# Performance work log

Measured on AMD Instinct MI355X. Metric: run time of the kernel, lower is better.

Reference implementation:

```python
import jax, jax.numpy as jnp
import numpy as np

B, N, FIN, HID, HEADS, LAYERS = 2048, 62, 128, 512, 8, 3
FOUT = HID // HEADS  # 64


def setup_inputs() -> dict:
    key = jax.random.key(0)
    ks = jax.random.split(key, 12)
    x = jax.random.normal(ks[0], (B, N, FIN), dtype=jnp.float32)
    adj = jax.random.randint(ks[1], (B, N, N), 0, 2, dtype=jnp.int32)
    # BatchNorm1d(62) params (eval mode, running stats)
    bn_gamma = jax.random.normal(ks[2], (N,), dtype=jnp.float32) * 0.1 + 1.0
    bn_beta = jax.random.normal(ks[3], (N,), dtype=jnp.float32) * 0.1
    bn_mean = jax.random.normal(ks[4], (N,), dtype=jnp.float32) * 0.1
    bn_var = jax.random.uniform(ks[5], (N,), dtype=jnp.float32, minval=0.5, maxval=1.5)
    # input MLP
    W_mlp = jax.random.normal(ks[6], (FIN, HID), dtype=jnp.float32) / np.sqrt(FIN)
    b_mlp = jnp.zeros((HID,), dtype=jnp.float32)
    # GAT params: one W [HID, FOUT] and one a [2*FOUT] per (layer, head)
    W_gat = jax.random.normal(ks[7], (LAYERS, HEADS, HID, FOUT), dtype=jnp.float32) / np.sqrt(HID)
    a_gat = jax.random.normal(ks[8], (LAYERS, HEADS, 2 * FOUT), dtype=jnp.float32) / np.sqrt(2 * FOUT)
    # output head
    W_out = jax.random.normal(ks[9], (HID, 3), dtype=jnp.float32) / np.sqrt(HID)
    b_out = jnp.zeros((3,), dtype=jnp.float32)
    return {
        "x": x, "adj": adj,
        "bn_gamma": bn_gamma, "bn_beta": bn_beta, "bn_mean": bn_mean, "bn_var": bn_var,
        "W_mlp": W_mlp, "b_mlp": b_mlp,
        "W_gat": W_gat, "a_gat": a_gat,
        "W_out": W_out, "b_out": b_out,
    }


def reference(x, adj, bn_gamma, bn_beta, bn_mean, bn_var, W_mlp, b_mlp, W_gat, a_gat, W_out, b_out):
    eps = 1e-5
    alpha = 0.2  # LeakyReLU slope
    # BatchNorm1d over the node dim (C=62), eval mode
    xb = (x - bn_mean[None, :, None]) * (bn_gamma / jnp.sqrt(bn_var + eps))[None, :, None] + bn_beta[None, :, None]
    h_x = xb @ W_mlp + b_mlp  # [B, N, HID]
    mask = adj > 0  # [B, N, N]
    n_layers, n_heads, _, f_out = W_gat.shape
    for l in range(n_layers):
        # all heads at once: h [H, B, N, FOUT]
        h = jnp.einsum('bnf,hfd->hbnd', h_x, W_gat[l])
        a1 = a_gat[l][:, :f_out]   # multiplies the repeat(1,N,1) part -> h_j
        a2 = a_gat[l][:, f_out:]   # multiplies the repeat(1,1,N) part -> h_i
        f1 = jnp.einsum('hbnd,hd->hbn', h, a1)  # per-node source term
        f2 = jnp.einsum('hbnd,hd->hbn', h, a2)  # per-node dest term
        # e[h,b,i,j] = leaky(a2.h_i + a1.h_j)  (matches cat/repeat layout)
        e = jax.nn.leaky_relu(f2[:, :, :, None] + f1[:, :, None, :], alpha)
        e = jnp.where(mask[None], e, jnp.float32(-9e15))
        # torch F.softmax(attention, dim=1) on [B,N,N] -> axis=2 here (the i axis)
        att = jax.nn.softmax(e, axis=2)
        hp = jnp.einsum('hbij,hbjd->hbid', att, h)
        hp = jax.nn.elu(hp)
        # concat heads on feature dim -> [B, N, HID]
        h_x = jnp.transpose(hp, (1, 2, 0, 3)).reshape(h_x.shape[0], h_x.shape[1], n_heads * f_out)
    pooled = jnp.sum(h_x, axis=1)  # [B, HID]
    logits = pooled @ W_out + b_out  # [B, 3]
    return jax.nn.log_softmax(logits, axis=-1)
```

## Files before the change

### kernel.cpp

```cpp
#include <hip/hip_runtime.h>
#include <cstdint>
#include <cstddef>

#define B_ 2048
#define N_ 62
#define FIN_ 128
#define HID_ 512
#define HEADS_ 8
#define FOUT_ 64
#define LAYERS_ 3
#define M_ (B_*N_)

typedef __bf16 bf16x8 __attribute__((ext_vector_type(8)));
typedef float  f32x4  __attribute__((ext_vector_type(4)));
typedef unsigned short u16;

#define LOG2E 1.4426950408889634f

#if __has_builtin(__builtin_amdgcn_exp2f)
#define EXP2F(x) __builtin_amdgcn_exp2f(x)
#else
#define EXP2F(x) exp2f(x)
#endif
#if __has_builtin(__builtin_amdgcn_logf)
#define LOG2F(x) __builtin_amdgcn_logf(x)
#else
#define LOG2F(x) log2f(x)
#endif

static __device__ __forceinline__ u16 f2bf(float f) {
    union { float f; uint32_t u; } v; v.f = f;
    uint32_t u = v.u;
    return (u16)((u + 0x7fffu + ((u >> 16) & 1u)) >> 16);
}
static __device__ __forceinline__ float bf2f(u16 s) {
    union { uint32_t u; float f; } v; v.u = ((uint32_t)s) << 16;
    return v.f;
}
static __device__ __forceinline__ float rdlane(float v, int l) {
    union { float f; int i; } a, b; a.f = v;
    b.i = __builtin_amdgcn_readlane(a.i, l);
    return b.f;
}

__global__ __launch_bounds__(256) void repack_w(
    const float* __restrict__ Wm, const float* __restrict__ Wg,
    const float* __restrict__ ag,
    u16* __restrict__ wmlp_t, u16* __restrict__ wgat2)
{
    int idx = blockIdx.x * 256 + threadIdx.x;
    const int T1 = HID_ * FIN_;
    const int T2 = LAYERS_ * HEADS_ * 80 * HID_;
    if (idx < T1) {
        int n = idx / FIN_, k = idx % FIN_;
        wmlp_t[idx] = f2bf(Wm[k * HID_ + n]);
    } else if (idx < T1 + T2) {
        int j = idx - T1;
        int lh = j / (80 * HID_);
        int r  = j % (80 * HID_);
        int n = r / HID_, k = r % HID_;
        float v;
        if (n < 64) {
            v = Wg[((size_t)lh * HID_ + k) * FOUT_ + n];
        } else if (n < 66) {
            const float* ap = ag + (size_t)lh * 128 + (n - 64) * 64;
            const float* wrow = Wg + ((size_t)lh * HID_ + k) * FOUT_;
            float s = 0.f;
            for (int d = 0; d < 64; d++) s += wrow[d] * ap[d];
            v = s * LOG2E;
        } else {
            v = 0.f;
        }
        wgat2[j] = f2bf(v);
    }
}

__global__ __launch_bounds__(256) void build_masks(
    const int* __restrict__ adj, uint64_t* __restrict__ masks,
    uint64_t* __restrict__ masksT)
{
    __shared__ uint32_t m32[128];
    const int b = blockIdx.x, tid = threadIdx.x;
    if (tid < 128) m32[tid] = 0;
    __syncthreads();
    const int* a = adj + (size_t)b * N_ * N_;
    for (int idx = tid; idx < N_ * N_; idx += 256) {
        int i = idx / N_, j = idx % N_;
        if (a[idx] > 0) atomicOr(&m32[i * 2 + (j >> 5)], 1u << (j & 31));
    }
    __syncthreads();
    if (tid < 128) ((uint32_t*)(masks + (size_t)b * 64))[tid] = m32[tid];
    if (tid < 64) {
        int j = tid;
        uint64_t c = 0;
        for (int i = 0; i < N_; i++) {
            uint64_t bit = (m32[i * 2 + (j >> 5)] >> (j & 31)) & 1u;
            c |= bit << i;
        }
        masksT[(size_t)b * 64 + j] = c;
    }
}

#define S_IN 520
#define S_T  72
#define S_X  136
#define X0   28160

__global__ __launch_bounds__(512, 4) void gat_fused(
    const float* __restrict__ x,
    const float* __restrict__ bng, const float* __restrict__ bnb,
    const float* __restrict__ bnm, const float* __restrict__ bnv,
    const u16* __restrict__ wmlp_t, const float* __restrict__ bm,
    const u16* __restrict__ wgat2,
    const uint64_t* __restrict__ masks, const uint64_t* __restrict__ masksT,
    const float* __restrict__ Wout, const float* __restrict__ bout,
    float* __restrict__ out)
{
    __shared__ __align__(16) u16 buf[36864];
    __shared__ uint64_t msk[64];
    __shared__ __align__(16) float fstat[1544];
    float* F1 = fstat;
    float* F2 = fstat + 512;
    float* LS = fstat + 1024;

    const int tid = threadIdx.x, b = blockIdx.x;
    const int wave = tid >> 6, lane = tid & 63;
    const int lr = lane & 15, lq = lane >> 4;
    const int w64 = wave * 64;

    const uint64_t cm = masksT[(size_t)b * 64 + lane];
    const uint32_t cml = (uint32_t)cm, cmh = (uint32_t)(cm >> 32);

    {
        const float* xg = x + (size_t)b * N_ * FIN_;
        for (int idx = tid; idx < 2048; idx += 512) {
            int n = idx >> 5, kq = idx & 31;
            ushort4 o = {0, 0, 0, 0};
            if (n < N_) {
                float s = bng[n] * rsqrtf(bnv[n] + 1e-5f);
                float sh = bnb[n] - bnm[n] * s;
                float4 v = *(const float4*)(xg + n * FIN_ + kq * 4);
                o.x = f2bf(v.x * s + sh); o.y = f2bf(v.y * s + sh);
                o.z = f2bf(v.z * s + sh); o.w = f2bf(v.w * s + sh);
            }
            *(ushort4*)&buf[X0 + n * S_X + kq * 4] = o;
        }
        if (tid < 64) msk[tid] = (tid < N_) ? masks[(size_t)b * 64 + tid] : 0ull;
    }
    __syncthreads();

    {
        f32x4 acc[4][4];
#pragma unroll
        for (int mt = 0; mt < 4; mt++)
#pragma unroll
            for (int nt = 0; nt < 4; nt++) acc[mt][nt] = (f32x4){0.f, 0.f, 0.f, 0.f};
        const int c0 = w64;
#pragma unroll
        for (int kt = 0; kt < 4; kt++) {
            int k0 = kt * 32;
            bf16x8 xf[4];
#pragma unroll
            for (int nt = 0; nt < 4; nt++)
                xf[nt] = *(const bf16x8*)&buf[X0 + (nt * 16 + lr) * S_X + k0 + lq * 8];
#pragma unroll
            for (int mt = 0; mt < 4; mt++) {
                bf16x8 wf = *(const bf16x8*)(wmlp_t + (size_t)(c0 + mt * 16 + lr) * FIN_ + k0 + lq * 8);
#pragma unroll
                for (int nt = 0; nt < 4; nt++)
                    acc[mt][nt] = __builtin_amdgcn_mfma_f32_16x16x32_bf16(
                        wf, xf[nt], acc[mt][nt], 0, 0, 0);
            }
        }
        __syncthreads();
        f32x4 bl[4];
#pragma unroll
        for (int mt = 0; mt < 4; mt++)
            bl[mt] = *(const f32x4*)&bm[c0 + mt * 16 + lq * 4];
#pragma unroll
        for (int mt = 0; mt < 4; mt++)
#pragma unroll
            for (int nt = 0; nt < 4; nt++) {
                int node = nt * 16 + lr;
                ushort4 pk;
                pk.x = f2bf(acc[mt][nt][0] + bl[mt][0]);
                pk.y = f2bf(acc[mt][nt][1] + bl[mt][1]);
                pk.z = f2bf(acc[mt][nt][2] + bl[mt][2]);
                pk.w = f2bf(acc[mt][nt][3] + bl[mt][3]);
                if (node < N_)
                    *(ushort4*)&buf[node * S_IN + c0 + mt * 16 + lq * 4] = pk;
            }
        if (lane < 16) {
            uint4 z = {0u, 0u, 0u, 0u};
            *(uint4*)&buf[(N_ + (lane >> 3)) * S_IN + c0 + (lane & 7) * 8] = z;
        }
    }
    __syncthreads();

#pragma unroll 1
    for (int l = 0; l < LAYERS_; l++) {
        const u16* wp = wgat2 + (size_t)(l * HEADS_ + wave) * 80 * HID_;

        {
            f32x4 accf[4];
#pragma unroll
            for (int mt = 0; mt < 4; mt++) accf[mt] = (f32x4){0.f, 0.f, 0.f, 0.f};
#pragma unroll 4
            for (int kt = 0; kt < 16; kt++) {
                int k0 = kt * 32;
                bf16x8 bfr = *(const bf16x8*)(wp + (size_t)(64 + lr) * HID_ + k0 + lq * 8);
#pragma unroll
                for (int mt = 0; mt < 4; mt++) {
                    bf16x8 af = *(const bf16x8*)&buf[(mt * 16 + lr) * S_IN + k0 + lq * 8];
                    accf[mt] = __builtin_amdgcn_mfma_f32_16x16x32_bf16(
                        af, bfr, accf[mt], 0, 0, 0);
                }
            }
            if (lr < 2) {
                float* Fp = lr ? F2 : F1;
#pragma unroll
                for (int mt = 0; mt < 4; mt++)
#pragma unroll
                    for (int r = 0; r < 4; r++)
                        Fp[w64 + mt * 16 + lq * 4 + r] = accf[mt][r];
            }
        }

        {
            float p1 = F1[w64 + lane];
            float p2 = F2[w64 + lane];
            float pm = (lane < N_) ? p2 : -3.0e38f;
#pragma unroll
            for (int off = 32; off; off >>= 1) pm = fmaxf(pm, __shfl_xor(pm, off, 64));
            float vm = pm + p1;
            float m = fmaxf(vm, 0.2f * vm);
            float s0 = 0.f, s1 = 0.f;
#pragma unroll
            for (int i = 0; i < N_; i += 2) {
                float fa = rdlane(p2, i), fb = rdlane(p2, i + 1);
                float va = fa + p1, vb = fb + p1;
                va = fmaxf(va, 0.2f * va); vb = fmaxf(vb, 0.2f * vb);
                float ea = EXP2F(va - m), eb = EXP2F(vb - m);
                uint32_t w = (i < 32) ? cml : cmh;
                s0 += ((w >> (i & 31)) & 1u) ? ea : 0.f;
                s1 += ((w >> ((i + 1) & 31)) & 1u) ? eb : 0.f;
            }
            float ssum = fmaxf(s0 + s1, 1e-35f);
            LS[w64 + lane] = m + LOG2F(ssum);
        }

        f32x4 acc[4][4];
#pragma unroll
        for (int mt = 0; mt < 4; mt++)
#pragma unroll
            for (int nt = 0; nt < 4; nt++) acc[mt][nt] = (f32x4){0.f, 0.f, 0.f, 0.f};
#pragma unroll 4
        for (int kt = 0; kt < 16; kt++) {
            int k0 = kt * 32;
            bf16x8 af[4];
#pragma unroll
            for (int mt = 0; mt < 4; mt++)
                af[mt] = *(const bf16x8*)&buf[(mt * 16 + lr) * S_IN + k0 + lq * 8];
#pragma unroll
            for (int nt = 0; nt < 4; nt++) {
                bf16x8 bfr = *(const bf16x8*)(wp + (size_t)(nt * 16 + lr) * HID_ + k0 + lq * 8);
#pragma unroll
                for (int mt = 0; mt < 4; mt++)
                    acc[mt][nt] = __builtin_amdgcn_mfma_f32_16x16x32_bf16(
                        af[mt], bfr, acc[mt][nt], 0, 0, 0);
            }
        }

        __syncthreads();

#pragma unroll
        for (int mt = 0; mt < 4; mt++)
#pragma unroll
            for (int nt = 0; nt < 4; nt++) {
                ushort4 pk;
                pk.x = f2bf(acc[mt][nt][0]); pk.y = f2bf(acc[mt][nt][1]);
                pk.z = f2bf(acc[mt][nt][2]); pk.w = f2bf(acc[mt][nt][3]);
                *(ushort4*)&buf[(w64 + nt * 16 + lr) * S_T + mt * 16 + lq * 4] = pk;
            }

        f32x4 acc2[4][4];
#pragma unroll
        for (int mt = 0; mt < 4; mt++)
#pragma unroll
            for (int it = 0; it < 4; it++) acc2[mt][it] = (f32x4){0.f, 0.f, 0.f, 0.f};
        float f2v[4];
#pragma unroll
        for (int it = 0; it < 4; it++) f2v[it] = F2[w64 + it * 16 + lr];
#pragma unroll
        for (int kt = 0; kt < 2; kt++) {
            int j0 = kt * 32 + lq * 8;
            bf16x8 pf[4];
            {
                f32x4 f1a = *(const f32x4*)&F1[w64 + j0];
                f32x4 f1b = *(const f32x4*)&F1[w64 + j0 + 4];
                f32x4 la  = *(const f32x4*)&LS[w64 + j0];
                f32x4 lb  = *(const f32x4*)&LS[w64 + j0 + 4];
#pragma unroll
                for (int it = 0; it < 4; it++) {
                    uint64_t mi = msk[it * 16 + lr];
                    uint32_t sh = (uint32_t)(mi >> (kt * 32)) >> (lq * 8);
#pragma unroll
                    for (int t = 0; t < 8; t++) {
                        float f1t = t < 4 ? f1a[t] : f1b[t - 4];
                        float lst = t < 4 ? la[t]  : lb[t - 4];
                        float v = f2v[it] + f1t;
                        v = fmaxf(v, 0.2f * v);
                        float p = EXP2F(v - lst);
                        p = ((sh >> t) & 1u) ? p : 0.f;
                        pf[it][t] = (__bf16)p;
                    }
                }
            }
#pragma unroll
            for (int mt = 0; mt < 4; mt++) {
                bf16x8 ha = *(const bf16x8*)&buf[(w64 + mt * 16 + lr) * S_T + kt * 32 + lq * 8];
#pragma unroll
                for (int it = 0; it < 4; it++)
                    acc2[mt][it] = __builtin_amdgcn_mfma_f32_16x16x32_bf16(
                        ha, pf[it], acc2[mt][it], 0, 0, 0);
            }
        }
        __syncthreads();

#pragma unroll
        for (int mt = 0; mt < 4; mt++)
#pragma unroll
            for (int it = 0; it < 4; it++) {
                int i = it * 16 + lr;
                ushort4 pk;
#pragma unroll
                for (int r = 0; r < 4; r++) {
                    float v = acc2[mt][it][r];
                    v = v > 0.f ? v : __expf(v) - 1.f;
                    ((u16*)&pk)[r] = f2bf(v);
                }
                if (i < N_)
                    *(ushort4*)&buf[i * S_IN + w64 + mt * 16 + lq * 4] = pk;
            }
        if (lane < 16) {
            uint4 z = {0u, 0u, 0u, 0u};
            *(uint4*)&buf[(N_ + (lane >> 3)) * S_IN + w64 + (lane & 7) * 8] = z;
        }
        __syncthreads();
    }

    {
        float s = 0.f;
#pragma unroll 2
        for (int n = 0; n < N_; n++) s += bf2f(buf[n * S_IN + tid]);
        fstat[tid] = s;
    }
    __syncthreads();
    if (tid < 192) {
        int c = tid >> 6, ln = tid & 63;
        float p = 0.f;
#pragma unroll
        for (int k = ln; k < HID_; k += 64) p += fstat[k] * Wout[k * 3 + c];
        for (int off = 32; off > 0; off >>= 1) p += __shfl_down(p, off, 64);
        if (ln == 0) fstat[1536 + c] = p + bout[c];
    }
    __syncthreads();
    if (tid == 0) {
        float l0 = fstat[1536], l1 = fstat[1537], l2 = fstat[1538];
        float mm = fmaxf(l0, fmaxf(l1, l2));
        float s = __expf(l0 - mm) + __expf(l1 - mm) + __expf(l2 - mm);
        float ls = mm + logf(s);
        out[b * 3 + 0] = l0 - ls;
        out[b * 3 + 1] = l1 - ls;
        out[b * 3 + 2] = l2 - ls;
    }
}

extern "C" void kernel_launch(void* const* d_in, const int* in_sizes, int n_in,
                              void* d_out, int out_size, void* d_ws, size_t ws_size,
                              hipStream_t stream)
{
    const float* x   = (const float*)d_in[0];
    const int*   adj = (const int*)d_in[1];
    const float* bng = (const float*)d_in[2];
    const float* bnb = (const float*)d_in[3];
    const float* bnm = (const float*)d_in[4];
    const float* bnv = (const float*)d_in[5];
    const float* Wm  = (const float*)d_in[6];
    const float* bm  = (const float*)d_in[7];
    const float* Wg  = (const float*)d_in[8];
    const float* ag  = (const float*)d_in[9];
    const float* Wo  = (const float*)d_in[10];
    const float* bo  = (const float*)d_in[11];
    float* out = (float*)d_out;

    uint64_t* masks  = (uint64_t*)d_ws;
    uint64_t* masksT = masks + (size_t)B_ * 64;
    u16* wmlp_t = (u16*)(masksT + (size_t)B_ * 64);
    u16* wgat2  = wmlp_t + (size_t)HID_ * FIN_;

    int rep_total = HID_ * FIN_ + LAYERS_ * HEADS_ * 80 * HID_;
    repack_w<<<(rep_total + 255) / 256, 256, 0, stream>>>(Wm, Wg, ag, wmlp_t, wgat2);
    build_masks<<<B_, 256, 0, stream>>>(adj, masks, masksT);

    gat_fused<<<B_, 512, 0, stream>>>(
        x, bng, bnb, bnm, bnv, wmlp_t, bm, wgat2,
        masks, masksT, Wo, bo, out);
}
```

Measured before the change: 727.8 us.

## Split activation buffer into per-wave regions and drop a block barrier

```diff
diff --git a/kernel.cpp b/kernel.cpp
--- a/kernel.cpp
+++ b/kernel.cpp
@@ -12,6 +12,7 @@
 #define M_ (B_*N_)
 
 typedef __bf16 bf16x8 __attribute__((ext_vector_type(8)));
+typedef __bf16 bf16x4 __attribute__((ext_vector_type(4)));
 typedef float  f32x4  __attribute__((ext_vector_type(4)));
 typedef unsigned short u16;
 
@@ -41,6 +42,12 @@
     union { float f; int i; } a, b; a.f = v;
     b.i = __builtin_amdgcn_readlane(a.i, l);
     return b.f;
+}
+static __device__ __forceinline__ bf16x4 pack4(f32x4 v) {
+    bf16x4 o;
+    o[0] = (__bf16)v[0]; o[1] = (__bf16)v[1];
+    o[2] = (__bf16)v[2]; o[3] = (__bf16)v[3];
+    return o;
 }
 
 __global__ __launch_bounds__(256) void repack_w(
@@ -101,10 +108,10 @@
     }
 }
 
-#define S_IN 520
-#define S_T  72
+#define S_R  72
+#define RSZ  4608
 #define S_X  136
-#define X0   28160
+#define X0   27648
 
 __global__ __launch_bounds__(512, 4) void gat_fused(
     const float* __restrict__ x,
@@ -127,6 +134,7 @@
     const int wave = tid >> 6, lane = tid & 63;
     const int lr = lane & 15, lq = lane >> 4;
     const int w64 = wave * 64;
+    const int wreg = wave * RSZ;
 
     const uint64_t cm = masksT[(size_t)b * 64 + lane];
     const uint32_t cml = (uint32_t)cm, cmh = (uint32_t)(cm >> 32);
@@ -135,15 +143,15 @@
         const float* xg = x + (size_t)b * N_ * FIN_;
         for (int idx = tid; idx < 2048; idx += 512) {
             int n = idx >> 5, kq = idx & 31;
-            ushort4 o = {0, 0, 0, 0};
+            bf16x4 o = {(__bf16)0.f, (__bf16)0.f, (__bf16)0.f, (__bf16)0.f};
             if (n < N_) {
                 float s = bng[n] * rsqrtf(bnv[n] + 1e-5f);
                 float sh = bnb[n] - bnm[n] * s;
                 float4 v = *(const float4*)(xg + n * FIN_ + kq * 4);
-                o.x = f2bf(v.x * s + sh); o.y = f2bf(v.y * s + sh);
-                o.z = f2bf(v.z * s + sh); o.w = f2bf(v.w * s + sh);
-            }
-            *(ushort4*)&buf[X0 + n * S_X + kq * 4] = o;
+                o[0] = (__bf16)(v.x * s + sh); o[1] = (__bf16)(v.y * s + sh);
+                o[2] = (__bf16)(v.z * s + sh); o[3] = (__bf16)(v.w * s + sh);
+            }
+            *(bf16x4*)&buf[X0 + n * S_X + kq * 4] = o;
         }
         if (tid < 64) msk[tid] = (tid < N_) ? masks[(size_t)b * 64 + tid] : 0ull;
     }
@@ -182,17 +190,13 @@
 #pragma unroll
             for (int nt = 0; nt < 4; nt++) {
                 int node = nt * 16 + lr;
-                ushort4 pk;
-                pk.x = f2bf(acc[mt][nt][0] + bl[mt][0]);
-                pk.y = f2bf(acc[mt][nt][1] + bl[mt][1]);
-                pk.z = f2bf(acc[mt][nt][2] + bl[mt][2]);
-                pk.w = f2bf(acc[mt][nt][3] + bl[mt][3]);
                 if (node < N_)
-                    *(ushort4*)&buf[node * S_IN + c0 + mt * 16 + lq * 4] = pk;
+                    *(bf16x4*)&buf[wreg + node * S_R + mt * 16 + lq * 4] =
+                        pack4(acc[mt][nt] + bl[mt]);
             }
         if (lane < 16) {
             uint4 z = {0u, 0u, 0u, 0u};
-            *(uint4*)&buf[(N_ + (lane >> 3)) * S_IN + c0 + (lane & 7) * 8] = z;
+            *(uint4*)&buf[wreg + (N_ + (lane >> 3)) * S_R + (lane & 7) * 8] = z;
         }
     }
     __syncthreads();
@@ -207,11 +211,11 @@
             for (int mt = 0; mt < 4; mt++) accf[mt] = (f32x4){0.f, 0.f, 0.f, 0.f};
 #pragma unroll 4
             for (int kt = 0; kt < 16; kt++) {
-                int k0 = kt * 32;
-                bf16x8 bfr = *(const bf16x8*)(wp + (size_t)(64 + lr) * HID_ + k0 + lq * 8);
+                int koff = (kt >> 1) * RSZ + (kt & 1) * 32 + lq * 8;
+                bf16x8 bfr = *(const bf16x8*)(wp + (size_t)(64 + lr) * HID_ + kt * 32 + lq * 8);
 #pragma unroll
                 for (int mt = 0; mt < 4; mt++) {
-                    bf16x8 af = *(const bf16x8*)&buf[(mt * 16 + lr) * S_IN + k0 + lq * 8];
+                    bf16x8 af = *(const bf16x8*)&buf[koff + (mt * 16 + lr) * S_R];
                     accf[mt] = __builtin_amdgcn_mfma_f32_16x16x32_bf16(
                         af, bfr, accf[mt], 0, 0, 0);
                 }
@@ -256,14 +260,14 @@
             for (int nt = 0; nt < 4; nt++) acc[mt][nt] = (f32x4){0.f, 0.f, 0.f, 0.f};
 #pragma unroll 4
         for (int kt = 0; kt < 16; kt++) {
-            int k0 = kt * 32;
+            int koff = (kt >> 1) * RSZ + (kt & 1) * 32 + lq * 8;
             bf16x8 af[4];
 #pragma unroll
             for (int mt = 0; mt < 4; mt++)
-                af[mt] = *(const bf16x8*)&buf[(mt * 16 + lr) * S_IN + k0 + lq * 8];
+                af[mt] = *(const bf16x8*)&buf[koff + (mt * 16 + lr) * S_R];
 #pragma unroll
             for (int nt = 0; nt < 4; nt++) {
-                bf16x8 bfr = *(const bf16x8*)(wp + (size_t)(nt * 16 + lr) * HID_ + k0 + lq * 8);
+                bf16x8 bfr = *(const bf16x8*)(wp + (size_t)(nt * 16 + lr) * HID_ + kt * 32 + lq * 8);
 #pragma unroll
                 for (int mt = 0; mt < 4; mt++)
                     acc[mt][nt] = __builtin_amdgcn_mfma_f32_16x16x32_bf16(
@@ -276,12 +280,9 @@
 #pragma unroll
         for (int mt = 0; mt < 4; mt++)
 #pragma unroll
-            for (int nt = 0; nt < 4; nt++) {
-                ushort4 pk;
-                pk.x = f2bf(acc[mt][nt][0]); pk.y = f2bf(acc[mt][nt][1]);
-                pk.z = f2bf(acc[mt][nt][2]); pk.w = f2bf(acc[mt][nt][3]);
-                *(ushort4*)&buf[(w64 + nt * 16 + lr) * S_T + mt * 16 + lq * 4] = pk;
-            }
+            for (int nt = 0; nt < 4; nt++)
+                *(bf16x4*)&buf[wreg + (nt * 16 + lr) * S_R + mt * 16 + lq * 4] =
+                    pack4(acc[mt][nt]);
 
         f32x4 acc2[4][4];
 #pragma unroll
@@ -295,56 +296,51 @@
         for (int kt = 0; kt < 2; kt++) {
             int j0 = kt * 32 + lq * 8;
             bf16x8 pf[4];
-            {
-                f32x4 f1a = *(const f32x4*)&F1[w64 + j0];
-                f32x4 f1b = *(const f32x4*)&F1[w64 + j0 + 4];
-                f32x4 la  = *(const f32x4*)&LS[w64 + j0];
-                f32x4 lb  = *(const f32x4*)&LS[w64 + j0 + 4];
+#pragma unroll
+            for (int h = 0; h < 2; h++) {
+                f32x4 f1h = *(const f32x4*)&F1[w64 + j0 + 4 * h];
+                f32x4 lsh = *(const f32x4*)&LS[w64 + j0 + 4 * h];
 #pragma unroll
                 for (int it = 0; it < 4; it++) {
                     uint64_t mi = msk[it * 16 + lr];
-                    uint32_t sh = (uint32_t)(mi >> (kt * 32)) >> (lq * 8);
-#pragma unroll
-                    for (int t = 0; t < 8; t++) {
-                        float f1t = t < 4 ? f1a[t] : f1b[t - 4];
-                        float lst = t < 4 ? la[t]  : lb[t - 4];
-                        float v = f2v[it] + f1t;
+                    uint32_t sh = ((uint32_t)(mi >> (kt * 32))) >> (lq * 8 + 4 * h);
+#pragma unroll
+                    for (int t = 0; t < 4; t++) {
+                        float v = f2v[it] + f1h[t];
                         v = fmaxf(v, 0.2f * v);
-                        float p = EXP2F(v - lst);
+                        float p = EXP2F(v - lsh[t]);
                         p = ((sh >> t) & 1u) ? p : 0.f;
-                        pf[it][t] = (__bf16)p;
+                        pf[it][4 * h + t] = (__bf16)p;
                     }
                 }
             }
 #pragma unroll
             for (int mt = 0; mt < 4; mt++) {
-                bf16x8 ha = *(const bf16x8*)&buf[(w64 + mt * 16 + lr) * S_T + kt * 32 + lq * 8];
+                bf16x8 ha = *(const bf16x8*)&buf[wreg + (mt * 16 + lr) * S_R + kt * 32 + lq * 8];
 #pragma unroll
                 for (int it = 0; it < 4; it++)
                     acc2[mt][it] = __builtin_amdgcn_mfma_f32_16x16x32_bf16(
                         ha, pf[it], acc2[mt][it], 0, 0, 0);
             }
         }
-        __syncthreads();
 
 #pragma unroll
         for (int mt = 0; mt < 4; mt++)
 #pragma unroll
             for (int it = 0; it < 4; it++) {
                 int i = it * 16 + lr;
-                ushort4 pk;
+                f32x4 e;
 #pragma unroll
                 for (int r = 0; r < 4; r++) {
                     float v = acc2[mt][it][r];
-                    v = v > 0.f ? v : __expf(v) - 1.f;
-                    ((u16*)&pk)[r] = f2bf(v);
+                    e[r] = v > 0.f ? v : EXP2F(v * LOG2E) - 1.f;
                 }
                 if (i < N_)
-                    *(ushort4*)&buf[i * S_IN + w64 + mt * 16 + lq * 4] = pk;
+                    *(bf16x4*)&buf[wreg + i * S_R + mt * 16 + lq * 4] = pack4(e);
             }
         if (lane < 16) {
             uint4 z = {0u, 0u, 0u, 0u};
-            *(uint4*)&buf[(N_ + (lane >> 3)) * S_IN + w64 + (lane & 7) * 8] = z;
+            *(uint4*)&buf[wreg + (N_ + (lane >> 3)) * S_R + (lane & 7) * 8] = z;
         }
         __syncthreads();
     }
@@ -352,7 +348,8 @@
     {
         float s = 0.f;
 #pragma unroll 2
-        for (int n = 0; n < N_; n++) s += bf2f(buf[n * S_IN + tid]);
+        for (int n = 0; n < N_; n++)
+            s += bf2f(buf[(tid >> 6) * RSZ + n * S_R + (tid & 63)]);
         fstat[tid] = s;
     }
     __syncthreads();
```

New measurement: 727.8 us. No clear change (+0.0%).
